# Optimization experiments

Measured on AMD Instinct MI355X. Metric: run time of the kernel, lower is better.

Reference implementation:

```python
import jax, jax.numpy as jnp
import numpy as np

N = 100000      # number of nodes (rows of sparse coef matrices)
D = 128         # embedding_size
E = 3200000     # nnz per sparse matrix (avg degree 32)
N_HGCN = 2      # n_hgcn_layers
N_LG = 2        # n_lg_layers


def spmm(rows, cols, vals, x, n_rows):
    # y[r] = sum_{k: rows[k]==r} vals[k] * x[cols[k]]  == sparse.mm(coef, x)
    return jax.ops.segment_sum(vals[:, None] * x[cols], rows, num_segments=n_rows)


def setup_inputs() -> dict:
    key = jax.random.key(0)
    ks = jax.random.split(key, 16)
    s = 1.0 / np.sqrt(D)
    inp = {
        "x": jax.random.normal(ks[0], (2, N, D), jnp.float32),
        "fusion_w1": jax.random.normal(ks[1], (D, D), jnp.float32) * s,
        "fusion_b1": jnp.zeros((D,), jnp.float32),
        "fusion_w2": jax.random.normal(ks[2], (D, 1), jnp.float32) * s,
        "fusion_b2": jnp.zeros((1,), jnp.float32),
        "hg_w": jax.random.normal(ks[3], (N_HGCN + 1, D, D), jnp.float32) * s,
        "lg_w": jax.random.normal(ks[4], (N_LG, D, D), jnp.float32) * s,
        "lg_b": jnp.zeros((N_LG, D), jnp.float32),
        "coef1_vals": jax.random.uniform(ks[5], (E,), jnp.float32) / 32.0,
        "coef2_vals": jax.random.uniform(ks[6], (E,), jnp.float32) / 32.0,
        "lg_vals": jax.random.uniform(ks[7], (E,), jnp.float32) / 32.0,
        "coef1_rows": jax.random.randint(ks[8], (E,), 0, N, jnp.int32),
        "coef1_cols": jax.random.randint(ks[9], (E,), 0, N, jnp.int32),
        "coef2_rows": jax.random.randint(ks[10], (E,), 0, N, jnp.int32),
        "coef2_cols": jax.random.randint(ks[11], (E,), 0, N, jnp.int32),
        "lg_rows": jax.random.randint(ks[12], (E,), 0, N, jnp.int32),
        "lg_cols": jax.random.randint(ks[13], (E,), 0, N, jnp.int32),
    }
    return inp


def reference(x, fusion_w1, fusion_b1, fusion_w2, fusion_b2, hg_w, lg_w, lg_b,
              coef1_vals, coef2_vals, lg_vals,
              coef1_rows, coef1_cols, coef2_rows, coef2_cols, lg_rows, lg_cols):
    # --- GatedFusionLayer (2 views -> softmax-gated sum over view axis) ---
    h1 = jnp.tanh(jnp.einsum('vnd,de->vne', x, fusion_w1) + fusion_b1)   # [2,N,D]
    score = jax.nn.softmax(h1 @ fusion_w2 + fusion_b2, axis=0)            # [2,N,1]
    fused = jnp.sum(x * score, axis=0)                                    # [N,D]

    # --- HypergraphConv: (linear -> spmm(coef1) -> relu) x (n_layers+1), final spmm(coef2) ---
    h = fused @ hg_w[0]
    h = jax.nn.relu(spmm(coef1_rows, coef1_cols, coef1_vals, h, N))
    for i in range(N_HGCN):
        # dropout is identity in eval mode
        h = h @ hg_w[i + 1]
        h = jax.nn.relu(spmm(coef1_rows, coef1_cols, coef1_vals, h, N))
    y = jax.nn.relu(spmm(coef2_rows, coef2_cols, coef2_vals, h, N))

    # --- LineConv: sum of input + n_lg_layers of (linear -> spmm(lg_coef)) ---
    acc = y
    cur = y
    for i in range(N_LG):
        cur = cur @ lg_w[i] + lg_b[i]
        cur = spmm(lg_rows, lg_cols, lg_vals, cur, N)
        acc = acc + cur

    # return (features_v, line-graph-fused features_u) concatenated -> [2N, D]
    return jnp.concatenate([h, acc], axis=0)
```

## Files before the change

kernel.cpp:

```cpp
#include <hip/hip_runtime.h>
#include <cmath>

#define TPB 256
#define CSH 10
#define CMAX 512
#define CHUNK 16384
#define TPB2 1024


__global__ void hist3_kernel(const int* __restrict__ r0, const int* __restrict__ r1,
                             const int* __restrict__ r2, int E, int N,
                             int* __restrict__ counts) {
  int i = blockIdx.x * TPB + threadIdx.x;
  if (i >= E) return;
  const int* rr = blockIdx.y == 0 ? r0 : blockIdx.y == 1 ? r1 : r2;
  atomicAdd(&counts[rr[i] + blockIdx.y * N], 1);
}

__global__ void scan1_kernel(const int* __restrict__ counts, int M,
                             int* __restrict__ P, int* __restrict__ S) {
  __shared__ int lds[TPB];
  int base = blockIdx.x * 2048 + threadIdx.x * 8;
  int v[8];
  int run = 0;
#pragma unroll
  for (int i = 0; i < 8; ++i) {
    int idx = base + i;
    int c = (idx < M) ? counts[idx] : 0;
    run += c;
    v[i] = run;
  }
  lds[threadIdx.x] = run;
  __syncthreads();
  for (int off = 1; off < TPB; off <<= 1) {
    int t = 0;
    if ((int)threadIdx.x >= off) t = lds[threadIdx.x - off];
    __syncthreads();
    if ((int)threadIdx.x >= off) lds[threadIdx.x] += t;
    __syncthreads();
  }
  int excl = (threadIdx.x > 0) ? lds[threadIdx.x - 1] : 0;
#pragma unroll
  for (int i = 0; i < 8; ++i) {
    int idx = base + i;
    if (idx < M) P[idx + 1] = v[i] + excl;
  }
  if (threadIdx.x == TPB - 1) S[blockIdx.x] = lds[TPB - 1];
}

__global__ void scan2_kernel(int* __restrict__ S, int NB) {
  __shared__ int lds[TPB];
  int carry = 0;
  for (int b0 = 0; b0 < NB; b0 += TPB) {
    int i = b0 + threadIdx.x;
    int val = (i < NB) ? S[i] : 0;
    lds[threadIdx.x] = val;
    __syncthreads();
    for (int off = 1; off < TPB; off <<= 1) {
      int t = 0;
      if ((int)threadIdx.x >= off) t = lds[threadIdx.x - off];
      __syncthreads();
      if ((int)threadIdx.x >= off) lds[threadIdx.x] += t;
      __syncthreads();
    }
    int inc = lds[threadIdx.x];
    int tot = lds[TPB - 1];
    if (i < NB) S[i] = inc + carry;
    carry += tot;
    __syncthreads();
  }
}

__global__ void scan3_kernel(int* __restrict__ P, const int* __restrict__ S, int M) {
  int b = blockIdx.x;
  int add = (b == 0) ? 0 : S[b - 1];
  int base = b * 2048;
  for (int i = threadIdx.x; i < 2048; i += TPB) {
    int idx = base + i;
    if (idx < M) P[idx + 1] += add;
  }
  if (b == 0 && threadIdx.x == 0) P[0] = 0;
}

__global__ void ccur_init_kernel(const int* __restrict__ P, int* __restrict__ ccur,
                                 int C, int M) {
  int c = blockIdx.x * TPB + threadIdx.x;
  if (c < C) {
    int r = c << CSH;
    ccur[c] = P[r < M ? r : M];
  }
}

__global__ __launch_bounds__(TPB) void binsort_kernel(
    const int* __restrict__ r0, const int* __restrict__ c0, const float* __restrict__ v0,
    const int* __restrict__ r1, const int* __restrict__ c1, const float* __restrict__ v1,
    const int* __restrict__ r2, const int* __restrict__ c2, const float* __restrict__ v2,
    int E, int N, int C, int* __restrict__ ccur, int2* __restrict__ stage) {
  __shared__ int hist[CMAX];
  int t0 = blockIdx.x * CHUNK;
  int t1 = t0 + CHUNK;
  int tot = 3 * E;
  if (t1 > tot) t1 = tot;
  for (int c = threadIdx.x; c < C; c += TPB) hist[c] = 0;
  __syncthreads();
  for (int t = t0 + (int)threadIdx.x; t < t1; t += TPB) {
    int m = (t >= 2 * E) ? 2 : (t >= E) ? 1 : 0;
    int i = t - m * E;
    const int* rr = m == 0 ? r0 : m == 1 ? r1 : r2;
    int gr = rr[i] + m * N;
    atomicAdd(&hist[gr >> CSH], 1);
  }
  __syncthreads();
  for (int c = threadIdx.x; c < C; c += TPB) {
    int h = hist[c];
    hist[c] = h ? atomicAdd(&ccur[c], h) : 0;
  }
  __syncthreads();
  for (int t = t0 + (int)threadIdx.x; t < t1; t += TPB) {
    int m = (t >= 2 * E) ? 2 : (t >= E) ? 1 : 0;
    int i = t - m * E;
    const int* rr = m == 0 ? r0 : m == 1 ? r1 : r2;
    const int* cc = m == 0 ? c0 : m == 1 ? c1 : c2;
    const float* vv = m == 0 ? v0 : m == 1 ? v1 : v2;
    int gr = rr[i] + m * N;
    int pos = atomicAdd(&hist[gr >> CSH], 1);
    stage[pos] = make_int2((cc[i] << CSH) | (gr & ((1 << CSH) - 1)),
                           __float_as_int(vv[i]));
  }
}

__global__ __launch_bounds__(TPB2) void csr_place2_kernel(
    const int* __restrict__ P, const int2* __restrict__ stage,
    int2* __restrict__ pairs, int M) {
  __shared__ int lcur[1 << CSH];
  int row0 = blockIdx.x << CSH;
  int row1 = row0 + (1 << CSH);
  if (row1 > M) row1 = M;
  for (int r = row0 + (int)threadIdx.x; r < row1; r += TPB2)
    lcur[r - row0] = P[r];
  __syncthreads();
  int start = P[row0], end = P[row1];
  for (int j = start + (int)threadIdx.x; j < end; j += TPB2) {
    int2 s = stage[j];
    int rl = s.x & ((1 << CSH) - 1);
    int col = ((unsigned)s.x) >> CSH;
    int pos = atomicAdd(&lcur[rl], 1);
    pairs[pos] = make_int2(col, s.y);
  }
}


__global__ __launch_bounds__(TPB) void gemm128_kernel(
    const float* __restrict__ A, const float* __restrict__ W,
    const float* __restrict__ bias, float* __restrict__ C, int nrows) {
  __shared__ float sW[64 * 128];
  const int cg = threadIdx.x & 15;
  const int rg = threadIdx.x >> 4;
  const int cA = cg * 4, cB = 64 + cg * 4;
  const int row0 = blockIdx.x * 128 + rg * 8;
  float acc[8][8];
#pragma unroll
  for (int j = 0; j < 8; ++j)
#pragma unroll
    for (int i = 0; i < 8; ++i) acc[j][i] = 0.f;

#pragma unroll 1
  for (int kc = 0; kc < 128; kc += 64) {
    for (int i = threadIdx.x * 4; i < 64 * 128; i += TPB * 4)
      *(float4*)&sW[i] = *(const float4*)&W[kc * 128 + i];
    __syncthreads();
#pragma unroll 1
    for (int k4 = 0; k4 < 64; k4 += 4) {
      float4 a[8];
#pragma unroll
      for (int j = 0; j < 8; ++j) {
        int r = row0 + j;
        a[j] = (r < nrows) ? *(const float4*)&A[(size_t)r * 128 + kc + k4]
                           : make_float4(0.f, 0.f, 0.f, 0.f);
      }
#pragma unroll
      for (int kk = 0; kk < 4; ++kk) {
        float4 w0 = *(const float4*)&sW[(k4 + kk) * 128 + cA];
        float4 w1 = *(const float4*)&sW[(k4 + kk) * 128 + cB];
#pragma unroll
        for (int j = 0; j < 8; ++j) {
          float aj = (kk == 0) ? a[j].x : (kk == 1) ? a[j].y : (kk == 2) ? a[j].z : a[j].w;
          acc[j][0] = fmaf(aj, w0.x, acc[j][0]);
          acc[j][1] = fmaf(aj, w0.y, acc[j][1]);
          acc[j][2] = fmaf(aj, w0.z, acc[j][2]);
          acc[j][3] = fmaf(aj, w0.w, acc[j][3]);
          acc[j][4] = fmaf(aj, w1.x, acc[j][4]);
          acc[j][5] = fmaf(aj, w1.y, acc[j][5]);
          acc[j][6] = fmaf(aj, w1.z, acc[j][6]);
          acc[j][7] = fmaf(aj, w1.w, acc[j][7]);
        }
      }
    }
    __syncthreads();
  }
  float bv[8];
  if (bias) {
    *(float4*)&bv[0] = *(const float4*)&bias[cA];
    *(float4*)&bv[4] = *(const float4*)&bias[cB];
  } else {
#pragma unroll
    for (int i = 0; i < 8; ++i) bv[i] = 0.f;
  }
#pragma unroll
  for (int j = 0; j < 8; ++j) {
    int r = row0 + j;
    if (r < nrows) {
      *(float4*)&C[(size_t)r * 128 + cA] =
          make_float4(acc[j][0] + bv[0], acc[j][1] + bv[1], acc[j][2] + bv[2], acc[j][3] + bv[3]);
      *(float4*)&C[(size_t)r * 128 + cB] =
          make_float4(acc[j][4] + bv[4], acc[j][5] + bv[5], acc[j][6] + bv[6], acc[j][7] + bv[7]);
    }
  }
}


__global__ __launch_bounds__(TPB) void fusion_score_kernel(
    const float* __restrict__ x, const float* __restrict__ W1,
    const float* __restrict__ b1, const float* __restrict__ w2,
    float* __restrict__ score, int nrows) {
  __shared__ float sW[64 * 128];
  const int v = blockIdx.y;
  const float* A = x + (size_t)v * nrows * 128;
  const int cg = threadIdx.x & 15;
  const int rg = threadIdx.x >> 4;
  const int cA = cg * 4, cB = 64 + cg * 4;
  const int row0 = blockIdx.x * 128 + rg * 8;
  float acc[8][8];
#pragma unroll
  for (int j = 0; j < 8; ++j)
#pragma unroll
    for (int i = 0; i < 8; ++i) acc[j][i] = 0.f;

#pragma unroll 1
  for (int kc = 0; kc < 128; kc += 64) {
    for (int i = threadIdx.x * 4; i < 64 * 128; i += TPB * 4)
      *(float4*)&sW[i] = *(const float4*)&W1[kc * 128 + i];
    __syncthreads();
#pragma unroll 1
    for (int k4 = 0; k4 < 64; k4 += 4) {
      float4 a[8];
#pragma unroll
      for (int j = 0; j < 8; ++j) {
        int r = row0 + j;
        a[j] = (r < nrows) ? *(const float4*)&A[(size_t)r * 128 + kc + k4]
                           : make_float4(0.f, 0.f, 0.f, 0.f);
      }
#pragma unroll
      for (int kk = 0; kk < 4; ++kk) {
        float4 w0 = *(const float4*)&sW[(k4 + kk) * 128 + cA];
        float4 w1 = *(const float4*)&sW[(k4 + kk) * 128 + cB];
#pragma unroll
        for (int j = 0; j < 8; ++j) {
          float aj = (kk == 0) ? a[j].x : (kk == 1) ? a[j].y : (kk == 2) ? a[j].z : a[j].w;
          acc[j][0] = fmaf(aj, w0.x, acc[j][0]);
          acc[j][1] = fmaf(aj, w0.y, acc[j][1]);
          acc[j][2] = fmaf(aj, w0.z, acc[j][2]);
          acc[j][3] = fmaf(aj, w0.w, acc[j][3]);
          acc[j][4] = fmaf(aj, w1.x, acc[j][4]);
          acc[j][5] = fmaf(aj, w1.y, acc[j][5]);
          acc[j][6] = fmaf(aj, w1.z, acc[j][6]);
          acc[j][7] = fmaf(aj, w1.w, acc[j][7]);
        }
      }
    }
    __syncthreads();
  }
  float bb[8], ww[8];
  *(float4*)&bb[0] = *(const float4*)&b1[cA];
  *(float4*)&bb[4] = *(const float4*)&b1[cB];
  *(float4*)&ww[0] = *(const float4*)&w2[cA];
  *(float4*)&ww[4] = *(const float4*)&w2[cB];
#pragma unroll
  for (int j = 0; j < 8; ++j) {
    float p = 0.f;
#pragma unroll
    for (int i = 0; i < 8; ++i) p += tanhf(acc[j][i] + bb[i]) * ww[i];
#pragma unroll
    for (int off = 8; off > 0; off >>= 1) p += __shfl_down(p, off, 16);
    if (cg == 0 && row0 + j < nrows) score[(size_t)v * nrows + row0 + j] = p;
  }
}

__global__ void combine_kernel(const float* __restrict__ x, const float* __restrict__ score,
                               float* __restrict__ fused, int nrows) {
  int i = blockIdx.x * TPB + threadIdx.x;
  if (i >= nrows * 32) return;
  int n = i >> 5;
  float s0 = score[n], s1 = score[nrows + n];
  float m = fmaxf(s0, s1);
  float e0 = expf(s0 - m), e1 = expf(s1 - m);
  float inv = 1.f / (e0 + e1);
  float w0 = e0 * inv, w1 = e1 * inv;
  float4 a = ((const float4*)x)[i];
  float4 b = ((const float4*)x)[(size_t)nrows * 32 + i];
  ((float4*)fused)[i] = make_float4(w0 * a.x + w1 * b.x, w0 * a.y + w1 * b.y,
                                    w0 * a.z + w1 * b.z, w0 * a.w + w1 * b.w);
}


__global__ __launch_bounds__(TPB) void spmm_kernel(
    const int* __restrict__ ptr, const int2* __restrict__ pairs,
    const float* __restrict__ x, float* __restrict__ y, int nrows, int do_relu,
    const float* __restrict__ add0, const float* __restrict__ add1) {
  int row = (blockIdx.x * TPB + threadIdx.x) >> 5;
  int hl = threadIdx.x & 31;
  if (row >= nrows) return;
  int start = ptr[row], end = ptr[row + 1];
  float ax = 0.f, ay = 0.f, az = 0.f, aw = 0.f;
  for (int j = start; j < end; j += 32) {
    int nrem = end - j;
    if (nrem > 32) nrem = 32;
    int2 pr = make_int2(0, 0);
    if (hl < nrem) pr = pairs[j + hl];
    for (int t = 0; t < nrem; ++t) {
      int c = __shfl(pr.x, t, 32);
      float v = __int_as_float(__shfl(pr.y, t, 32));
      const float4 xv = *(const float4*)&x[(size_t)c * 128 + hl * 4];
      ax = fmaf(v, xv.x, ax);
      ay = fmaf(v, xv.y, ay);
      az = fmaf(v, xv.z, az);
      aw = fmaf(v, xv.w, aw);
    }
  }
  if (do_relu) {
    ax = fmaxf(ax, 0.f); ay = fmaxf(ay, 0.f);
    az = fmaxf(az, 0.f); aw = fmaxf(aw, 0.f);
  }
  size_t o = (size_t)row * 128 + hl * 4;
  if (add0) { float4 t = *(const float4*)&add0[o]; ax += t.x; ay += t.y; az += t.z; aw += t.w; }
  if (add1) { float4 t = *(const float4*)&add1[o]; ax += t.x; ay += t.y; az += t.z; aw += t.w; }
  *(float4*)&y[o] = make_float4(ax, ay, az, aw);
}


extern "C" void kernel_launch(void* const* d_in, const int* in_sizes, int n_in,
                              void* d_out, int out_size, void* d_ws, size_t ws_size,
                              hipStream_t stream) {
  const float* x   = (const float*)d_in[0];
  const float* fw1 = (const float*)d_in[1];
  const float* fb1 = (const float*)d_in[2];
  const float* fw2 = (const float*)d_in[3];
  const float* hgw = (const float*)d_in[5];
  const float* lgw = (const float*)d_in[6];
  const float* lgb = (const float*)d_in[7];
  const float* c1v = (const float*)d_in[8];
  const float* c2v = (const float*)d_in[9];
  const float* lgv = (const float*)d_in[10];
  const int* c1r = (const int*)d_in[11];
  const int* c1c = (const int*)d_in[12];
  const int* c2r = (const int*)d_in[13];
  const int* c2c = (const int*)d_in[14];
  const int* lgr = (const int*)d_in[15];
  const int* lgc = (const int*)d_in[16];

  const int N = in_sizes[0] / 256;
  const int E = in_sizes[8];
  const int M = 3 * N;
  const int C = (M + (1 << CSH) - 1) >> CSH;

  char* ws = (char*)d_ws;
  size_t off = 0;
  auto alloc = [&](size_t bytes) -> void* {
    void* p = ws + off;
    off += (bytes + 511) & ~(size_t)511;
    return p;
  };
  int* P      = (int*)alloc((size_t)(M + 1) * 4);
  int* S      = (int*)alloc((size_t)4096 * 4);
  int* counts = (int*)alloc((size_t)M * 4);
  int* ccur   = (int*)alloc((size_t)(C + 1) * 4);
  int2* pairs = (int2*)alloc((size_t)3 * E * 8);
  float* score = (float*)alloc((size_t)2 * N * 4);
  float* Fbase = (float*)alloc((size_t)3 * N * 128 * 4);
  float* F0 = Fbase;
  float* F1 = Fbase + (size_t)N * 128;
  float* F2 = Fbase + (size_t)2 * N * 128;
  int2* stage = (int2*)Fbase;
  float* outH = (float*)d_out;
  float* outA = (float*)d_out + (size_t)N * 128;

  hipMemsetAsync(counts, 0, (size_t)M * 4, stream);
  int gE = (E + TPB - 1) / TPB;
  dim3 g3(gE, 3);
  hist3_kernel<<<g3, TPB, 0, stream>>>(c1r, c2r, lgr, E, N, counts);
  int NB = (M + 2047) / 2048;
  scan1_kernel<<<NB, TPB, 0, stream>>>(counts, M, P, S);
  scan2_kernel<<<1, TPB, 0, stream>>>(S, NB);
  scan3_kernel<<<NB, TPB, 0, stream>>>(P, S, M);
  ccur_init_kernel<<<(C + TPB - 1) / TPB, TPB, 0, stream>>>(P, ccur, C, M);
  int NBS = (3 * E + CHUNK - 1) / CHUNK;
  binsort_kernel<<<NBS, TPB, 0, stream>>>(c1r, c1c, c1v, c2r, c2c, c2v,
                                          lgr, lgc, lgv, E, N, C, ccur, stage);
  csr_place2_kernel<<<C, TPB2, 0, stream>>>(P, stage, pairs, M);

  dim3 gf((N + 127) / 128, 2);
  fusion_score_kernel<<<gf, TPB, 0, stream>>>(x, fw1, fb1, fw2, score, N);
  combine_kernel<<<(N * 32 + TPB - 1) / TPB, TPB, 0, stream>>>(x, score, F0, N);

  int gg = (N + 127) / 128;
  int gs = (N + 7) / 8;

  gemm128_kernel<<<gg, TPB, 0, stream>>>(F0, hgw + 0 * 16384, nullptr, F1, N);
  spmm_kernel<<<gs, TPB, 0, stream>>>(P, pairs, F1, F2, N, 1, nullptr, nullptr);
  gemm128_kernel<<<gg, TPB, 0, stream>>>(F2, hgw + 1 * 16384, nullptr, F1, N);
  spmm_kernel<<<gs, TPB, 0, stream>>>(P, pairs, F1, F2, N, 1, nullptr, nullptr);
  gemm128_kernel<<<gg, TPB, 0, stream>>>(F2, hgw + 2 * 16384, nullptr, F1, N);
  spmm_kernel<<<gs, TPB, 0, stream>>>(P, pairs, F1, outH, N, 1, nullptr, nullptr);
  spmm_kernel<<<gs, TPB, 0, stream>>>(P + N, pairs, outH, F0, N, 1, nullptr, nullptr);

  gemm128_kernel<<<gg, TPB, 0, stream>>>(F0, lgw + 0 * 16384, lgb + 0, F1, N);
  spmm_kernel<<<gs, TPB, 0, stream>>>(P + 2 * N, pairs, F1, F2, N, 0, nullptr, nullptr);
  gemm128_kernel<<<gg, TPB, 0, stream>>>(F2, lgw + 1 * 16384, lgb + 128, F1, N);
  spmm_kernel<<<gs, TPB, 0, stream>>>(P + 2 * N, pairs, F1, outA, N, 0, F0, F2);
}
```

Baseline: 2.999 ms.

## Build CSR row pointers from coarse bucket counts instead of fine histogram

Replaces the per-row global-atomic histogram and three-pass multi-block scan with a coarse per-bucket count done in shared memory, a single-block scan over buckets, and per-bucket row counting and scanning inside the placement kernel, which now also writes the row pointer array. This removes global atomics on 300K counters and several small kernel launches. In exchange the placement kernel reads the staged entries twice, and the single-block bucket scan only works while the bucket count fits in 1024 threads.

```diff
diff --git a/kernel.cpp b/kernel.cpp
--- a/kernel.cpp
+++ b/kernel.cpp
@@ -8,87 +8,46 @@
 #define TPB2 1024
 
 
-__global__ void hist3_kernel(const int* __restrict__ r0, const int* __restrict__ r1,
-                             const int* __restrict__ r2, int E, int N,
-                             int* __restrict__ counts) {
-  int i = blockIdx.x * TPB + threadIdx.x;
-  if (i >= E) return;
-  const int* rr = blockIdx.y == 0 ? r0 : blockIdx.y == 1 ? r1 : r2;
-  atomicAdd(&counts[rr[i] + blockIdx.y * N], 1);
-}
-
-__global__ void scan1_kernel(const int* __restrict__ counts, int M,
-                             int* __restrict__ P, int* __restrict__ S) {
-  __shared__ int lds[TPB];
-  int base = blockIdx.x * 2048 + threadIdx.x * 8;
-  int v[8];
-  int run = 0;
-#pragma unroll
-  for (int i = 0; i < 8; ++i) {
-    int idx = base + i;
-    int c = (idx < M) ? counts[idx] : 0;
-    run += c;
-    v[i] = run;
-  }
-  lds[threadIdx.x] = run;
-  __syncthreads();
-  for (int off = 1; off < TPB; off <<= 1) {
-    int t = 0;
-    if ((int)threadIdx.x >= off) t = lds[threadIdx.x - off];
-    __syncthreads();
-    if ((int)threadIdx.x >= off) lds[threadIdx.x] += t;
-    __syncthreads();
-  }
-  int excl = (threadIdx.x > 0) ? lds[threadIdx.x - 1] : 0;
-#pragma unroll
-  for (int i = 0; i < 8; ++i) {
-    int idx = base + i;
-    if (idx < M) P[idx + 1] = v[i] + excl;
-  }
-  if (threadIdx.x == TPB - 1) S[blockIdx.x] = lds[TPB - 1];
-}
-
-__global__ void scan2_kernel(int* __restrict__ S, int NB) {
-  __shared__ int lds[TPB];
-  int carry = 0;
-  for (int b0 = 0; b0 < NB; b0 += TPB) {
-    int i = b0 + threadIdx.x;
-    int val = (i < NB) ? S[i] : 0;
-    lds[threadIdx.x] = val;
-    __syncthreads();
-    for (int off = 1; off < TPB; off <<= 1) {
-      int t = 0;
-      if ((int)threadIdx.x >= off) t = lds[threadIdx.x - off];
-      __syncthreads();
-      if ((int)threadIdx.x >= off) lds[threadIdx.x] += t;
-      __syncthreads();
-    }
-    int inc = lds[threadIdx.x];
-    int tot = lds[TPB - 1];
-    if (i < NB) S[i] = inc + carry;
-    carry += tot;
-    __syncthreads();
-  }
-}
-
-__global__ void scan3_kernel(int* __restrict__ P, const int* __restrict__ S, int M) {
-  int b = blockIdx.x;
-  int add = (b == 0) ? 0 : S[b - 1];
-  int base = b * 2048;
-  for (int i = threadIdx.x; i < 2048; i += TPB) {
-    int idx = base + i;
-    if (idx < M) P[idx + 1] += add;
-  }
-  if (b == 0 && threadIdx.x == 0) P[0] = 0;
-}
-
-__global__ void ccur_init_kernel(const int* __restrict__ P, int* __restrict__ ccur,
-                                 int C, int M) {
-  int c = blockIdx.x * TPB + threadIdx.x;
-  if (c < C) {
-    int r = c << CSH;
-    ccur[c] = P[r < M ? r : M];
-  }
+__global__ __launch_bounds__(TPB) void coarse_count_kernel(
+    const int* __restrict__ r0, const int* __restrict__ r1,
+    const int* __restrict__ r2, int E, int N, int C, int* __restrict__ Cc) {
+  __shared__ int hist[CMAX];
+  int tot = 3 * E;
+  int t0 = blockIdx.x * CHUNK;
+  int t1 = t0 + CHUNK;
+  if (t1 > tot) t1 = tot;
+  for (int c = threadIdx.x; c < C; c += TPB) hist[c] = 0;
+  __syncthreads();
+  for (int t = t0 + (int)threadIdx.x; t < t1; t += TPB) {
+    int m = (t >= 2 * E) ? 2 : (t >= E) ? 1 : 0;
+    int i = t - m * E;
+    const int* rr = m == 0 ? r0 : m == 1 ? r1 : r2;
+    atomicAdd(&hist[(rr[i] + m * N) >> CSH], 1);
+  }
+  __syncthreads();
+  for (int c = threadIdx.x; c < C; c += TPB) {
+    int h = hist[c];
+    if (h) atomicAdd(&Cc[c], h);
+  }
+}
+
+__global__ __launch_bounds__(TPB2) void scanC_kernel(
+    const int* __restrict__ Cc, int* __restrict__ Pc, int* __restrict__ ccur, int C) {
+  __shared__ int lds[TPB2];
+  int tid = threadIdx.x;
+  int v = (tid < C) ? Cc[tid] : 0;
+  lds[tid] = v;
+  __syncthreads();
+  for (int off = 1; off < TPB2; off <<= 1) {
+    int t = (tid >= off) ? lds[tid - off] : 0;
+    __syncthreads();
+    if (tid >= off) lds[tid] += t;
+    __syncthreads();
+  }
+  int incl = lds[tid];
+  int excl = incl - v;
+  if (tid < C) { Pc[tid] = excl; ccur[tid] = excl; }
+  if (tid == C - 1) Pc[C] = incl;
 }
 
 __global__ __launch_bounds__(TPB) void binsort_kernel(
@@ -129,23 +88,36 @@
   }
 }
 
-__global__ __launch_bounds__(TPB2) void csr_place2_kernel(
-    const int* __restrict__ P, const int2* __restrict__ stage,
-    int2* __restrict__ pairs, int M) {
-  __shared__ int lcur[1 << CSH];
-  int row0 = blockIdx.x << CSH;
-  int row1 = row0 + (1 << CSH);
-  if (row1 > M) row1 = M;
-  for (int r = row0 + (int)threadIdx.x; r < row1; r += TPB2)
-    lcur[r - row0] = P[r];
-  __syncthreads();
-  int start = P[row0], end = P[row1];
-  for (int j = start + (int)threadIdx.x; j < end; j += TPB2) {
+__global__ __launch_bounds__(TPB2) void csr_place3_kernel(
+    const int* __restrict__ Pc, const int2* __restrict__ stage,
+    int2* __restrict__ pairs, int* __restrict__ P, int M, int C) {
+  __shared__ int h[1 << CSH];
+  const int tid = threadIdx.x;
+  const int row0 = blockIdx.x << CSH;
+  const int start = Pc[blockIdx.x], end = Pc[blockIdx.x + 1];
+  h[tid] = 0;
+  __syncthreads();
+  for (int j = start + tid; j < end; j += TPB2)
+    atomicAdd(&h[stage[j].x & ((1 << CSH) - 1)], 1);
+  __syncthreads();
+  int cnt = h[tid];
+  for (int off = 1; off < TPB2; off <<= 1) {
+    int t = (tid >= off) ? h[tid - off] : 0;
+    __syncthreads();
+    if (tid >= off) h[tid] += t;
+    __syncthreads();
+  }
+  int cur = start + (h[tid] - cnt);
+  int row = row0 + tid;
+  if (row < M) P[row] = cur;
+  if (blockIdx.x == C - 1 && tid == 0) P[M] = end;
+  h[tid] = cur;
+  __syncthreads();
+  for (int j = start + tid; j < end; j += TPB2) {
     int2 s = stage[j];
     int rl = s.x & ((1 << CSH) - 1);
-    int col = ((unsigned)s.x) >> CSH;
-    int pos = atomicAdd(&lcur[rl], 1);
-    pairs[pos] = make_int2(col, s.y);
+    int pos = atomicAdd(&h[rl], 1);
+    pairs[pos] = make_int2(((unsigned)s.x) >> CSH, s.y);
   }
 }
 
@@ -371,8 +343,8 @@
     return p;
   };
   int* P      = (int*)alloc((size_t)(M + 1) * 4);
-  int* S      = (int*)alloc((size_t)4096 * 4);
-  int* counts = (int*)alloc((size_t)M * 4);
+  int* Cc     = (int*)alloc((size_t)(C + 1) * 4);
+  int* Pc     = (int*)alloc((size_t)(C + 1) * 4);
   int* ccur   = (int*)alloc((size_t)(C + 1) * 4);
   int2* pairs = (int2*)alloc((size_t)3 * E * 8);
   float* score = (float*)alloc((size_t)2 * N * 4);
@@ -384,19 +356,13 @@
   float* outH = (float*)d_out;
   float* outA = (float*)d_out + (size_t)N * 128;
 
-  hipMemsetAsync(counts, 0, (size_t)M * 4, stream);
-  int gE = (E + TPB - 1) / TPB;
-  dim3 g3(gE, 3);
-  hist3_kernel<<<g3, TPB, 0, stream>>>(c1r, c2r, lgr, E, N, counts);
-  int NB = (M + 2047) / 2048;
-  scan1_kernel<<<NB, TPB, 0, stream>>>(counts, M, P, S);
-  scan2_kernel<<<1, TPB, 0, stream>>>(S, NB);
-  scan3_kernel<<<NB, TPB, 0, stream>>>(P, S, M);
-  ccur_init_kernel<<<(C + TPB - 1) / TPB, TPB, 0, stream>>>(P, ccur, C, M);
+  hipMemsetAsync(Cc, 0, (size_t)(C + 1) * 4, stream);
   int NBS = (3 * E + CHUNK - 1) / CHUNK;
+  coarse_count_kernel<<<NBS, TPB, 0, stream>>>(c1r, c2r, lgr, E, N, C, Cc);
+  scanC_kernel<<<1, TPB2, 0, stream>>>(Cc, Pc, ccur, C);
   binsort_kernel<<<NBS, TPB, 0, stream>>>(c1r, c1c, c1v, c2r, c2c, c2v,
                                           lgr, lgc, lgv, E, N, C, ccur, stage);
-  csr_place2_kernel<<<C, TPB2, 0, stream>>>(P, stage, pairs, M);
+  csr_place3_kernel<<<C, TPB2, 0, stream>>>(Pc, stage, pairs, P, M, C);
 
   dim3 gf((N + 127) / 128, 2);
   fusion_score_kernel<<<gf, TPB, 0, stream>>>(x, fw1, fb1, fw2, score, N);
```

Result: faster. 2.626 ms (-12.4%).
